# Optimization experiments

Measured on AMD Instinct MI355X. Metric: run time of the kernel, lower is better.

Reference implementation:

```python
import jax, jax.numpy as jnp
import numpy as np

DIM = 512  # DIM_IMAGE_EMBEDDING
HEAD = 64
B, T = 16, 2048


def setup_inputs() -> dict:
    key = jax.random.key(0)
    ks = jax.random.split(key, 8)
    s = 1.0 / np.sqrt(DIM)
    return {
        'x': jax.random.normal(ks[0], (B, T, DIM), jnp.float32),
        'Wq': jax.random.normal(ks[1], (HEAD, DIM), jnp.float32) * s,
        'Wk': jax.random.normal(ks[2], (HEAD, DIM), jnp.float32) * s,
        'Wv': jax.random.normal(ks[3], (HEAD, DIM), jnp.float32) * s,
        'fx_real': jax.random.normal(ks[4], (T, HEAD // 4), jnp.float32),
        'fx_imag': jax.random.normal(ks[5], (T, HEAD // 4), jnp.float32),
        'fy_real': jax.random.normal(ks[6], (T, HEAD // 4), jnp.float32),
        'fy_imag': jax.random.normal(ks[7], (T, HEAD // 4), jnp.float32),
    }


def _rotate_half(t, fr, fi):
    # t: [B, T, H/2] viewed as H/4 complex pairs; fr, fi: [T, H/4]
    b, s, d = t.shape
    tc = t.reshape(b, s, d // 2, 2)
    a, bb = tc[..., 0], tc[..., 1]
    ro = a * fr - bb * fi  # real part of complex product
    io = a * fi + bb * fr  # imag part
    return jnp.stack([ro, io], axis=-1).reshape(b, s, d)


def apply_rotary_2d(t, fx_real, fx_imag, fy_real, fy_imag):
    h = t.shape[-1] // 2
    vx = _rotate_half(t[..., :h], fx_real, fx_imag)
    vy = _rotate_half(t[..., h:], fy_real, fy_imag)
    return jnp.concatenate([vx, vy], axis=-1)


def reference(x, Wq, Wk, Wv, fx_real, fx_imag, fy_real, fy_imag):
    C = x.shape[-1]
    q = jnp.einsum('btc,hc->bth', x, Wq)
    k = jnp.einsum('btc,hc->bth', x, Wk)
    v = jnp.einsum('btc,hc->bth', x, Wv)
    q = apply_rotary_2d(q, fx_real, fx_imag, fy_real, fy_imag)
    k = apply_rotary_2d(k, fx_real, fx_imag, fy_real, fy_imag)
    # NOTE: original scales by input dim C (=512), not head_size
    wei = jnp.einsum('bqh,bkh->bqk', q, k) / jnp.sqrt(jnp.float32(C))
    softwei = jax.nn.softmax(wei, axis=-1)
    out = jnp.einsum('bqk,bkh->bqh', softwei, v)
    return out
```

## Files before the change

kernel.cpp:

```cpp
#include <hip/hip_runtime.h>
#include <hip/hip_bf16.h>

#define BB 16
#define TT 2048
#define DIMC 512
#define HEADH 64

typedef __attribute__((ext_vector_type(8))) short short8v;
typedef __attribute__((ext_vector_type(4))) float f32x4;

static __device__ __forceinline__ unsigned short f2bf(float f) {
    __hip_bfloat16 h = __float2bfloat16(f);
    unsigned short u;
    __builtin_memcpy(&u, &h, 2);
    return u;
}
static __device__ __forceinline__ unsigned int packbf(float lo, float hi) {
    float2 f2; f2.x = lo; f2.y = hi;
    __hip_bfloat162 h2 = __float22bfloat162_rn(f2);
    unsigned int u;
    __builtin_memcpy(&u, &h2, 4);
    return u;
}
#define EXP2R __builtin_amdgcn_exp2f
static __device__ __forceinline__ void async_copy16(void* lds, const void* g) {
    __builtin_amdgcn_global_load_lds(
        (const __attribute__((address_space(1))) unsigned char*)g,
        (__attribute__((address_space(3))) unsigned char*)lds, 16, 0, 0);
}

union bfrag {
    unsigned int u[4];
    short8v v;
};

__global__ __launch_bounds__(256) void wcvt_kernel(
    const float* __restrict__ Wq, const float* __restrict__ Wk,
    const float* __restrict__ Wv, unsigned short* __restrict__ wb)
{
    const int idx = blockIdx.x * 256 + threadIdx.x;
    const int e   = idx << 3;
    const int row = e >> 9, col = e & 511;
    const float* src = (row < 64) ? Wq : (row < 128) ? Wk : Wv;
    const float* p = src + (size_t)(row & 63) * DIMC + col;
    float4 a = *(const float4*)p;
    float4 b = *(const float4*)(p + 4);
    uint4 o;
    o.x = packbf(a.x, a.y); o.y = packbf(a.z, a.w);
    o.z = packbf(b.x, b.y); o.w = packbf(b.z, b.w);
    *(uint4*)(wb + e) = o;
}

__global__ __launch_bounds__(256, 2) void qkv_mfma_kernel(
    const float* __restrict__ x,
    const unsigned short* __restrict__ wb,
    const float* __restrict__ fxr, const float* __restrict__ fxi,
    const float* __restrict__ fyr, const float* __restrict__ fyi,
    unsigned short* __restrict__ qo, unsigned short* __restrict__ ko,
    unsigned short* __restrict__ vt)
{
    __shared__ unsigned char xlds[16384];

    const int tid = threadIdx.x;
    const int w   = tid >> 6;
    const int l   = tid & 63;
    const int q   = l & 15;
    const int g   = l >> 4;
    const int t0  = blockIdx.x << 6;

    f32x4 acc[3][4];
    #pragma unroll
    for (int j = 0; j < 3; ++j)
        #pragma unroll
        for (int tt = 0; tt < 4; ++tt) acc[j][tt] = (f32x4){0.f, 0.f, 0.f, 0.f};

    const unsigned short* wp0 = wb + ((size_t)((3 * w + 0) * 16 + q)) * DIMC + 8 * g;
    const unsigned short* wp1 = wb + ((size_t)((3 * w + 1) * 16 + q)) * DIMC + 8 * g;
    const unsigned short* wp2 = wb + ((size_t)((3 * w + 2) * 16 + q)) * DIMC + 8 * g;

    const int rl = l >> 3;
    const int cb = (l & 7) ^ rl;
    const float* xsrc0 = x + (size_t)(t0 + 16 * w + 0 + rl) * DIMC + 4 * cb;
    const float* xsrc1 = x + (size_t)(t0 + 16 * w + 8 + rl) * DIMC + 4 * cb;
    unsigned char* xdst0 = xlds + (16 * w + 0) * 128;
    unsigned char* xdst1 = xlds + (16 * w + 8) * 128;

#define STAGE_X(bufsel, k0) do {                                              \
        async_copy16(xdst0 + (bufsel) * 8192, xsrc0 + (k0));                  \
        async_copy16(xdst1 + (bufsel) * 8192, xsrc1 + (k0));                  \
    } while (0)

    STAGE_X(0, 0);
    __syncthreads();

    int cur = 0;
    for (int it = 0; it < 16; ++it) {
        const int k0 = it << 5;
        if (it < 15) STAGE_X(cur ^ 1, k0 + 32);

        short8v wf0 = *(const short8v*)(wp0 + k0);
        short8v wf1 = *(const short8v*)(wp1 + k0);
        short8v wf2 = *(const short8v*)(wp2 + k0);

        const unsigned char* xb = xlds + cur * 8192;
        #pragma unroll
        for (int tt = 0; tt < 4; ++tt) {
            const int rr = tt * 16 + q;
            const int s0 = (2 * g)     ^ (q & 7);
            const int s1 = (2 * g + 1) ^ (q & 7);
            float4 f0 = *(const float4*)(xb + rr * 128 + s0 * 16);
            float4 f1 = *(const float4*)(xb + rr * 128 + s1 * 16);
            bfrag xv;
            xv.u[0] = packbf(f0.x, f0.y); xv.u[1] = packbf(f0.z, f0.w);
            xv.u[2] = packbf(f1.x, f1.y); xv.u[3] = packbf(f1.z, f1.w);
            acc[0][tt] = __builtin_amdgcn_mfma_f32_16x16x32_bf16(wf0, xv.v, acc[0][tt], 0, 0, 0);
            acc[1][tt] = __builtin_amdgcn_mfma_f32_16x16x32_bf16(wf1, xv.v, acc[1][tt], 0, 0, 0);
            acc[2][tt] = __builtin_amdgcn_mfma_f32_16x16x32_bf16(wf2, xv.v, acc[2][tt], 0, 0, 0);
        }

        __syncthreads();
        cur ^= 1;
    }

    const float qscale = 1.4426950408889634f / 22.627416997969522f;
    #pragma unroll
    for (int j = 0; j < 3; ++j) {
        const int gt   = 3 * w + j;
        const int mat  = gt >> 2;
        const int hbase = (gt & 3) * 16 + 4 * g;
        #pragma unroll
        for (int tt = 0; tt < 4; ++tt) {
            const int trow = t0 + tt * 16 + q;
            const int tl   = trow & (TT - 1);
            if (mat == 2) {
                const int b = trow >> 11;
                #pragma unroll
                for (int r = 0; r < 4; ++r)
                    vt[((size_t)(b * HEADH) + hbase + r) * TT + tl] = f2bf(acc[j][tt][r]);
            } else {
                const float sc = (mat == 0) ? qscale : 1.f;
                unsigned short* dst = ((mat == 0) ? qo : ko) + (size_t)trow * HEADH;
                const int half = hbase >> 5;
                const float* frt = half ? fyr : fxr;
                const float* fit = half ? fyi : fxi;
                const int pi0 = (hbase & 31) >> 1;
                float fr0 = frt[tl * 16 + pi0],     fi0 = fit[tl * 16 + pi0];
                float fr1 = frt[tl * 16 + pi0 + 1], fi1 = fit[tl * 16 + pi0 + 1];
                float e0 = acc[j][tt][0] * fr0 - acc[j][tt][1] * fi0;
                float e1 = acc[j][tt][0] * fi0 + acc[j][tt][1] * fr0;
                float e2 = acc[j][tt][2] * fr1 - acc[j][tt][3] * fi1;
                float e3 = acc[j][tt][2] * fi1 + acc[j][tt][3] * fr1;
                uint2 ow;
                ow.x = packbf(e0 * sc, e1 * sc);
                ow.y = packbf(e2 * sc, e3 * sc);
                *(uint2*)(dst + hbase) = ow;
            }
        }
    }
#undef STAGE_X
}

__global__ __launch_bounds__(1024, 4) void attn_mfma_kernel(
    const unsigned short* __restrict__ qws,
    const unsigned short* __restrict__ kws,
    const unsigned short* __restrict__ vtw,
    float* __restrict__ out)
{
    __shared__ unsigned char smem[98304];

    const int tid = threadIdx.x;
    const int w   = tid >> 6;
    const int wq  = w & 7;
    const int h   = w >> 3;
    const int l   = tid & 63;
    const int q   = l & 15;
    const int g   = l >> 4;
    const int b   = blockIdx.x >> 4;
    const int q0  = (blockIdx.x & 15) << 7;
    const int qw  = q0 + 16 * wq;
    const int rx  = q & 7;
    const int swz = (q & 7) << 2;

    const int rl = l >> 3;
    const int sl = (l & 7) ^ rl;

    unsigned int* pldsw = (unsigned int*)(smem + 65536 + (w << 11));

    const unsigned short* kbase = kws + (size_t)b * TT * HEADH;
    const unsigned short* vbase = vtw + (size_t)b * HEADH * TT;

    const unsigned short* ksrc = kbase + (size_t)(h * 1024 + 8 * wq + rl) * HEADH + 8 * sl;
    const unsigned short* vsrc = vbase + (size_t)(8 * wq + rl) * TT + h * 1024 + 8 * sl;

#define STAGE_TILE(bufsel, kv)  do {                                          \
        unsigned char* kd = smem + (h << 14) + (bufsel) * 8192 + (wq << 10);  \
        async_copy16(kd, ksrc + (size_t)(kv) * HEADH);                        \
        unsigned char* vd = smem + 32768 + (h << 14) + (bufsel) * 8192 + (wq << 10); \
        async_copy16(vd, vsrc + (kv));                                        \
    } while (0)

    short8v qf0, qf1;
    {
        const unsigned short* qp = qws + ((size_t)(b * TT + qw + q)) * HEADH + 8 * g;
        qf0 = *(const short8v*)(qp);
        qf1 = *(const short8v*)(qp + 32);
    }

    f32x4 oacc[4];
    #pragma unroll
    for (int mt = 0; mt < 4; ++mt) oacc[mt] = (f32x4){0.f, 0.f, 0.f, 0.f};
    float m = -1e30f, lsum = 0.f;

    STAGE_TILE(0, 0);
    __syncthreads();

    int cur = 0;
    for (int it = 0; it < 16; ++it) {
        const int kv0 = it << 6;
        if (it < 15) STAGE_TILE(cur ^ 1, kv0 + 64);

        const unsigned char* kb = smem + (h << 14) + cur * 8192;
        const unsigned char* vb = smem + 32768 + (h << 14) + cur * 8192;

        f32x4 sacc[4];
        #pragma unroll
        for (int n = 0; n < 4; ++n) {
            const int r = 16 * n + q;
            const short8v k0 = *(const short8v*)(kb + r * 128 + ((g ^ rx) << 4));
            const short8v k1 = *(const short8v*)(kb + r * 128 + (((4 + g) ^ rx) << 4));
            f32x4 z = (f32x4){0.f, 0.f, 0.f, 0.f};
            z = __builtin_amdgcn_mfma_f32_16x16x32_bf16(k0, qf0, z, 0, 0, 0);
            z = __builtin_amdgcn_mfma_f32_16x16x32_bf16(k1, qf1, z, 0, 0, 0);
            sacc[n] = z;
        }

        float nx[4];
        #pragma unroll
        for (int n = 0; n < 4; ++n)
            nx[n] = fmaxf(fmaxf(sacc[n][0], sacc[n][1]),
                          fmaxf(sacc[n][2], sacc[n][3]));
        float cmax = fmaxf(fmaxf(nx[0], nx[1]), fmaxf(nx[2], nx[3]));
        cmax = fmaxf(cmax, __shfl_xor(cmax, 16));
        cmax = fmaxf(cmax, __shfl_xor(cmax, 32));
        const float mnew = fmaxf(m, cmax);

        float p[4][4];
        #pragma unroll
        for (int n = 0; n < 4; ++n) {
            #pragma unroll
            for (int r = 0; r < 4; ++r)
                p[n][r] = EXP2R(sacc[n][r] - mnew);
            uint2 wv;
            wv.x = packbf(p[n][0], p[n][1]);
            wv.y = packbf(p[n][2], p[n][3]);
            *(uint2*)&pldsw[q * 32 + ((8 * n + 2 * g) ^ swz)] = wv;
        }

        const float sc = EXP2R(m - mnew);
        if (__any(cmax > m)) {
            #pragma unroll
            for (int mt = 0; mt < 4; ++mt)
                #pragma unroll
                for (int r = 0; r < 4; ++r) oacc[mt][r] *= sc;
        }

        #pragma unroll
        for (int s = 0; s < 2; ++s) {
            const short8v pb = *(const short8v*)&pldsw[q * 32 + ((16 * s + 4 * g) ^ swz)];
            #pragma unroll
            for (int mt = 0; mt < 4; ++mt) {
                const int d = 16 * mt + q;
                const short8v vfr = *(const short8v*)(vb + d * 128 + ((((s << 2) + g) ^ rx) << 4));
                oacc[mt] = __builtin_amdgcn_mfma_f32_16x16x32_bf16(vfr, pb, oacc[mt], 0, 0, 0);
            }
        }

        float psum = 0.f;
        #pragma unroll
        for (int n = 0; n < 4; ++n)
            #pragma unroll
            for (int r = 0; r < 4; ++r) psum += p[n][r];
        psum += __shfl_xor(psum, 16);
        psum += __shfl_xor(psum, 32);
        lsum = lsum * sc + psum;
        m = mnew;

        __syncthreads();
        cur ^= 1;
    }

    __syncthreads();
    float* o_f  = (float*)smem;
    float* ml_f = (float*)(smem + 65536);
    {
        const int prow = h * 128 + 16 * wq + q;
        #pragma unroll
        for (int mt = 0; mt < 4; ++mt)
            *(f32x4*)&o_f[prow * 64 + 16 * mt + 4 * g] = oacc[mt];
        if (g == 0) {
            ml_f[h * 256 + 16 * wq + q]       = m;
            ml_f[h * 256 + 128 + 16 * wq + q] = lsum;
        }
    }
    __syncthreads();

    const int cq = tid >> 3;
    const int ch = (tid & 7) << 3;
    const float m0 = ml_f[cq],       l0 = ml_f[128 + cq];
    const float m1 = ml_f[256 + cq], l1 = ml_f[384 + cq];
    const float M  = fmaxf(m0, m1);
    const float a0 = EXP2R(m0 - M), a1 = EXP2R(m1 - M);
    const float inv = 1.f / (a0 * l0 + a1 * l1);
    const float* o0 = &o_f[cq * 64 + ch];
    const float* o1 = &o_f[(128 + cq) * 64 + ch];
    float4 A0 = *(const float4*)(o0), B0 = *(const float4*)(o0 + 4);
    float4 A1 = *(const float4*)(o1), B1 = *(const float4*)(o1 + 4);
    float* op = out + ((size_t)(b * TT + q0 + cq)) * HEADH + ch;
    *(float4*)(op)     = make_float4((a0 * A0.x + a1 * A1.x) * inv,
                                     (a0 * A0.y + a1 * A1.y) * inv,
                                     (a0 * A0.z + a1 * A1.z) * inv,
                                     (a0 * A0.w + a1 * A1.w) * inv);
    *(float4*)(op + 4) = make_float4((a0 * B0.x + a1 * B1.x) * inv,
                                     (a0 * B0.y + a1 * B1.y) * inv,
                                     (a0 * B0.z + a1 * B1.z) * inv,
                                     (a0 * B0.w + a1 * B1.w) * inv);
#undef STAGE_TILE
}

extern "C" void kernel_launch(void* const* d_in, const int* in_sizes, int n_in,
                              void* d_out, int out_size, void* d_ws, size_t ws_size,
                              hipStream_t stream)
{
    const float* x   = (const float*)d_in[0];
    const float* Wq  = (const float*)d_in[1];
    const float* Wk  = (const float*)d_in[2];
    const float* Wv  = (const float*)d_in[3];
    const float* fxr = (const float*)d_in[4];
    const float* fxi = (const float*)d_in[5];
    const float* fyr = (const float*)d_in[6];
    const float* fyi = (const float*)d_in[7];
    float* out = (float*)d_out;

    unsigned short* qo = (unsigned short*)d_ws;
    unsigned short* ko = qo + (size_t)BB * TT * HEADH;
    unsigned short* vt = ko + (size_t)BB * TT * HEADH;
    unsigned short* wb = vt + (size_t)BB * TT * HEADH;

    wcvt_kernel<<<48, 256, 0, stream>>>(Wq, Wk, Wv, wb);
    qkv_mfma_kernel<<<(BB * TT) / 64, 256, 0, stream>>>(x, wb, fxr, fxi, fyr, fyi,
                                                        qo, ko, vt);
    attn_mfma_kernel<<<BB * 16, 1024, 0, stream>>>(qo, ko, vt, out);
}
```

Measured before the change: 65.46 us.

## Split K across two wave groups in QKV projection with LDS reduction

```diff
diff --git a/kernel.cpp b/kernel.cpp
--- a/kernel.cpp
+++ b/kernel.cpp
@@ -51,7 +51,7 @@
     *(uint4*)(wb + e) = o;
 }
 
-__global__ __launch_bounds__(256, 2) void qkv_mfma_kernel(
+__global__ __launch_bounds__(512, 4) void qkv_mfma_kernel(
     const float* __restrict__ x,
     const unsigned short* __restrict__ wb,
     const float* __restrict__ fxr, const float* __restrict__ fxi,
@@ -59,10 +59,12 @@
     unsigned short* __restrict__ qo, unsigned short* __restrict__ ko,
     unsigned short* __restrict__ vt)
 {
-    __shared__ unsigned char xlds[16384];
+    __shared__ unsigned char smem[81920];
 
     const int tid = threadIdx.x;
     const int w   = tid >> 6;
+    const int grp = w >> 2;
+    const int w4  = w & 3;
     const int l   = tid & 63;
     const int q   = l & 15;
     const int g   = l >> 4;
@@ -74,16 +76,16 @@
         #pragma unroll
         for (int tt = 0; tt < 4; ++tt) acc[j][tt] = (f32x4){0.f, 0.f, 0.f, 0.f};
 
-    const unsigned short* wp0 = wb + ((size_t)((3 * w + 0) * 16 + q)) * DIMC + 8 * g;
-    const unsigned short* wp1 = wb + ((size_t)((3 * w + 1) * 16 + q)) * DIMC + 8 * g;
-    const unsigned short* wp2 = wb + ((size_t)((3 * w + 2) * 16 + q)) * DIMC + 8 * g;
+    const unsigned short* wp0 = wb + ((size_t)((3 * w4 + 0) * 16 + q)) * DIMC + 256 * grp + 8 * g;
+    const unsigned short* wp1 = wb + ((size_t)((3 * w4 + 1) * 16 + q)) * DIMC + 256 * grp + 8 * g;
+    const unsigned short* wp2 = wb + ((size_t)((3 * w4 + 2) * 16 + q)) * DIMC + 256 * grp + 8 * g;
 
     const int rl = l >> 3;
     const int cb = (l & 7) ^ rl;
-    const float* xsrc0 = x + (size_t)(t0 + 16 * w + 0 + rl) * DIMC + 4 * cb;
-    const float* xsrc1 = x + (size_t)(t0 + 16 * w + 8 + rl) * DIMC + 4 * cb;
-    unsigned char* xdst0 = xlds + (16 * w + 0) * 128;
-    unsigned char* xdst1 = xlds + (16 * w + 8) * 128;
+    const float* xsrc0 = x + (size_t)(t0 + 16 * w4 + 0 + rl) * DIMC + 256 * grp + 4 * cb;
+    const float* xsrc1 = x + (size_t)(t0 + 16 * w4 + 8 + rl) * DIMC + 256 * grp + 4 * cb;
+    unsigned char* xdst0 = smem + grp * 16384 + (16 * w4 + 0) * 128;
+    unsigned char* xdst1 = smem + grp * 16384 + (16 * w4 + 8) * 128;
 
 #define STAGE_X(bufsel, k0) do {                                              \
         async_copy16(xdst0 + (bufsel) * 8192, xsrc0 + (k0));                  \
@@ -94,15 +96,15 @@
     __syncthreads();
 
     int cur = 0;
-    for (int it = 0; it < 16; ++it) {
+    for (int it = 0; it < 8; ++it) {
         const int k0 = it << 5;
-        if (it < 15) STAGE_X(cur ^ 1, k0 + 32);
+        if (it < 7) STAGE_X(cur ^ 1, k0 + 32);
 
         short8v wf0 = *(const short8v*)(wp0 + k0);
         short8v wf1 = *(const short8v*)(wp1 + k0);
         short8v wf2 = *(const short8v*)(wp2 + k0);
 
-        const unsigned char* xb = xlds + cur * 8192;
+        const unsigned char* xb = smem + grp * 16384 + cur * 8192;
         #pragma unroll
         for (int tt = 0; tt < 4; ++tt) {
             const int rr = tt * 16 + q;
@@ -122,10 +124,29 @@
         cur ^= 1;
     }
 
+    float* o_f = (float*)(smem + 32768);
+    if (grp == 1) {
+        #pragma unroll
+        for (int j = 0; j < 3; ++j)
+            #pragma unroll
+            for (int tt = 0; tt < 4; ++tt)
+                *(f32x4*)&o_f[(((3 * w4 + j) * 4 + tt) * 64 + l) * 4] = acc[j][tt];
+    }
+    __syncthreads();
+    if (grp == 1) return;
+    #pragma unroll
+    for (int j = 0; j < 3; ++j)
+        #pragma unroll
+        for (int tt = 0; tt < 4; ++tt) {
+            f32x4 o = *(const f32x4*)&o_f[(((3 * w4 + j) * 4 + tt) * 64 + l) * 4];
+            #pragma unroll
+            for (int r = 0; r < 4; ++r) acc[j][tt][r] += o[r];
+        }
+
     const float qscale = 1.4426950408889634f / 22.627416997969522f;
     #pragma unroll
     for (int j = 0; j < 3; ++j) {
-        const int gt   = 3 * w + j;
+        const int gt   = 3 * w4 + j;
         const int mat  = gt >> 2;
         const int hbase = (gt & 3) * 16 + 4 * g;
         #pragma unroll
@@ -347,7 +368,7 @@
     unsigned short* wb = vt + (size_t)BB * TT * HEADH;
 
     wcvt_kernel<<<48, 256, 0, stream>>>(Wq, Wk, Wv, wb);
-    qkv_mfma_kernel<<<(BB * TT) / 64, 256, 0, stream>>>(x, wb, fxr, fxi, fyr, fyi,
+    qkv_mfma_kernel<<<(BB * TT) / 64, 512, 0, stream>>>(x, wb, fxr, fxi, fyr, fyi,
                                                         qo, ko, vt);
     attn_mfma_kernel<<<BB * 16, 1024, 0, stream>>>(qo, ko, vt, out);
 }
```

Measured after the change: 65.72 us. Within noise of the previous version (+0.4%).

## Load full 32-row x tile into LDS at once, drop per-step double buffering

Applied to the files above, without the earlier changes.

```diff
diff --git a/kernel.cpp b/kernel.cpp
--- a/kernel.cpp
+++ b/kernel.cpp
@@ -59,57 +59,49 @@
     unsigned short* __restrict__ qo, unsigned short* __restrict__ ko,
     unsigned short* __restrict__ vt)
 {
-    __shared__ unsigned char xlds[16384];
+    __shared__ unsigned char xlds[65536];
 
     const int tid = threadIdx.x;
     const int w   = tid >> 6;
     const int l   = tid & 63;
     const int q   = l & 15;
     const int g   = l >> 4;
-    const int t0  = blockIdx.x << 6;
-
-    f32x4 acc[3][4];
+    const int t0  = blockIdx.x << 5;
+
+    #pragma unroll
+    for (int c = 0; c < 16; ++c) {
+        const int rc = 8 * w + (c >> 1);
+        const int hc = c & 1;
+        const float* src = x + (size_t)(t0 + rc) * DIMC
+                             + 4 * (64 * hc + (l ^ (rc & 7)));
+        async_copy16(xlds + rc * 2048 + hc * 1024, src);
+    }
+    __syncthreads();
+
+    f32x4 acc[3][2];
     #pragma unroll
     for (int j = 0; j < 3; ++j)
         #pragma unroll
-        for (int tt = 0; tt < 4; ++tt) acc[j][tt] = (f32x4){0.f, 0.f, 0.f, 0.f};
+        for (int tt = 0; tt < 2; ++tt) acc[j][tt] = (f32x4){0.f, 0.f, 0.f, 0.f};
 
     const unsigned short* wp0 = wb + ((size_t)((3 * w + 0) * 16 + q)) * DIMC + 8 * g;
     const unsigned short* wp1 = wb + ((size_t)((3 * w + 1) * 16 + q)) * DIMC + 8 * g;
     const unsigned short* wp2 = wb + ((size_t)((3 * w + 2) * 16 + q)) * DIMC + 8 * g;
 
-    const int rl = l >> 3;
-    const int cb = (l & 7) ^ rl;
-    const float* xsrc0 = x + (size_t)(t0 + 16 * w + 0 + rl) * DIMC + 4 * cb;
-    const float* xsrc1 = x + (size_t)(t0 + 16 * w + 8 + rl) * DIMC + 4 * cb;
-    unsigned char* xdst0 = xlds + (16 * w + 0) * 128;
-    unsigned char* xdst1 = xlds + (16 * w + 8) * 128;
-
-#define STAGE_X(bufsel, k0) do {                                              \
-        async_copy16(xdst0 + (bufsel) * 8192, xsrc0 + (k0));                  \
-        async_copy16(xdst1 + (bufsel) * 8192, xsrc1 + (k0));                  \
-    } while (0)
-
-    STAGE_X(0, 0);
-    __syncthreads();
-
-    int cur = 0;
-    for (int it = 0; it < 16; ++it) {
-        const int k0 = it << 5;
-        if (it < 15) STAGE_X(cur ^ 1, k0 + 32);
-
+    #pragma unroll 4
+    for (int kc = 0; kc < 16; ++kc) {
+        const int k0 = kc << 5;
         short8v wf0 = *(const short8v*)(wp0 + k0);
         short8v wf1 = *(const short8v*)(wp1 + k0);
         short8v wf2 = *(const short8v*)(wp2 + k0);
 
-        const unsigned char* xb = xlds + cur * 8192;
-        #pragma unroll
-        for (int tt = 0; tt < 4; ++tt) {
+        #pragma unroll
+        for (int tt = 0; tt < 2; ++tt) {
             const int rr = tt * 16 + q;
-            const int s0 = (2 * g)     ^ (q & 7);
-            const int s1 = (2 * g + 1) ^ (q & 7);
-            float4 f0 = *(const float4*)(xb + rr * 128 + s0 * 16);
-            float4 f1 = *(const float4*)(xb + rr * 128 + s1 * 16);
+            const int s0 = (8 * kc + 2 * g)     ^ (q & 7);
+            const int s1 = (8 * kc + 2 * g + 1) ^ (q & 7);
+            float4 f0 = *(const float4*)(xlds + rr * 2048 + s0 * 16);
+            float4 f1 = *(const float4*)(xlds + rr * 2048 + s1 * 16);
             bfrag xv;
             xv.u[0] = packbf(f0.x, f0.y); xv.u[1] = packbf(f0.z, f0.w);
             xv.u[2] = packbf(f1.x, f1.y); xv.u[3] = packbf(f1.z, f1.w);
@@ -117,9 +109,6 @@
             acc[1][tt] = __builtin_amdgcn_mfma_f32_16x16x32_bf16(wf1, xv.v, acc[1][tt], 0, 0, 0);
             acc[2][tt] = __builtin_amdgcn_mfma_f32_16x16x32_bf16(wf2, xv.v, acc[2][tt], 0, 0, 0);
         }
-
-        __syncthreads();
-        cur ^= 1;
     }
 
     const float qscale = 1.4426950408889634f / 22.627416997969522f;
@@ -129,7 +118,7 @@
         const int mat  = gt >> 2;
         const int hbase = (gt & 3) * 16 + 4 * g;
         #pragma unroll
-        for (int tt = 0; tt < 4; ++tt) {
+        for (int tt = 0; tt < 2; ++tt) {
             const int trow = t0 + tt * 16 + q;
             const int tl   = trow & (TT - 1);
             if (mat == 2) {
@@ -157,7 +146,6 @@
             }
         }
     }
-#undef STAGE_X
 }
 
 __global__ __launch_bounds__(1024, 4) void attn_mfma_kernel(
@@ -347,7 +335,7 @@
     unsigned short* wb = vt + (size_t)BB * TT * HEADH;
 
     wcvt_kernel<<<48, 256, 0, stream>>>(Wq, Wk, Wv, wb);
-    qkv_mfma_kernel<<<(BB * TT) / 64, 256, 0, stream>>>(x, wb, fxr, fxi, fyr, fyi,
+    qkv_mfma_kernel<<<(BB * TT) / 32, 256, 0, stream>>>(x, wb, fxr, fxi, fyr, fyi,
                                                         qo, ko, vt);
     attn_mfma_kernel<<<BB * 16, 1024, 0, stream>>>(qo, ko, vt, out);
 }
```

New measurement: 76.17 us. 1.16x slower.
